# Performance work log

Hardware: AMD Instinct MI355X
Metric: run time of the kernel (lower is better)

Reference implementation:

```python
import jax, jax.numpy as jnp
import numpy as np

B, NF, G, F, D = 8192, 128, 16, 8, 512


def setup_inputs() -> dict:
    key = jax.random.key(0)
    k1, k2, k3, k4 = jax.random.split(key, 4)
    x = jax.random.normal(k1, (B, NF), dtype=jnp.float32)
    # per-group Linear weights: torch Linear(F, D) weight is [D, F]; store as [G, F, D]
    # init scale ~ 1/sqrt(fan_in) like torch default
    W = jax.random.normal(k2, (G, F, D), dtype=jnp.float32) / np.sqrt(F)
    b = jax.random.normal(k3, (G, D), dtype=jnp.float32) / np.sqrt(F)
    group_idx = jnp.arange(G * F, dtype=jnp.int64).reshape(G, F)  # contiguous groups
    masked_group_idx = jax.random.randint(k4, (B,), 0, G, dtype=jnp.int64)
    return {"x": x, "W": W, "b": b, "group_idx": group_idx,
            "masked_group_idx": masked_group_idx}


def reference(x, W, b, group_idx, masked_group_idx):
    # gather each group's feature columns: [B, G, F]
    xg = x[:, group_idx]
    # batched small GEMMs (block-diagonal gather-GEMM) + bias: [B, G, D]
    out = jnp.einsum('bgf,gfd->bgd', xg, W) + b[None, :, :]
    # zero out the masked group token per batch row
    mask = masked_group_idx[:, None] == jnp.arange(out.shape[1])[None, :]  # [B, G]
    out = jnp.where(mask[:, :, None], jnp.zeros((), out.dtype), out)
    return out
```

## Files before the change

### kernel.cpp

```cpp
#include <hip/hip_runtime.h>
#include <stdint.h>

constexpr int kB  = 8192;
constexpr int kNF = 128;
constexpr int kG  = 16;
constexpr int kF  = 8;
constexpr int kD  = 512;
constexpr int R   = 32;
constexpr int THREADS = 1024;
constexpr int BLOCKS  = kB / R;

typedef float f32x4 __attribute__((ext_vector_type(4)));

__global__ __launch_bounds__(THREADS) void ge_kernel(
    const float* __restrict__ x,
    const float* __restrict__ W,
    const float* __restrict__ bias,
    const int*  __restrict__ mgi_w,
    float* __restrict__ out)
{
    __shared__ __align__(16) float xs[R][kNF];
    __shared__ int mg[R];

    const int tid = threadIdx.x;
    const int b0  = blockIdx.x * R;

    const int lane = tid & 63;
    const int probe = mgi_w[lane];
    const bool lane_ok = (lane & 1) ? (probe == 0)
                                    : (probe >= 0 && probe < kG);
    const bool is64 = (__ballot(lane_ok) == ~0ull);

    {
        const f32x4* xsrc = (const f32x4*)(x + (size_t)b0 * kNF);
        ((f32x4*)&xs[0][0])[tid] = xsrc[tid];
    }
    if (tid < R) mg[tid] = mgi_w[is64 ? 2 * (b0 + tid) : (b0 + tid)];

    const int hi   = tid >> 7;
    const int dcol = (tid & 127) << 2;

    float w[2][kF][4];
    float bz[2][4];
    #pragma unroll
    for (int q = 0; q < 2; ++q) {
        const int g = 8 * q + hi;
        #pragma unroll
        for (int f = 0; f < kF; ++f)
            *(f32x4*)w[q][f] =
                *(const f32x4*)(W + (size_t)(g * kF + f) * kD + dcol);
        *(f32x4*)bz[q] = *(const f32x4*)(bias + (size_t)g * kD + dcol);
    }

    __syncthreads();

    float* outp = out + (size_t)b0 * (kG * kD) + dcol;

    #pragma unroll 1
    for (int r = 0; r < R; ++r) {
        const int m = mg[r];
        const float* xrow = &xs[r][0];
        float* orow = outp + (size_t)r * (kG * kD);
        #pragma unroll
        for (int q = 0; q < 2; ++q) {
            const int g = 8 * q + hi;
            const f32x4 xv0 = *(const f32x4*)&xrow[g * kF];
            const f32x4 xv1 = *(const f32x4*)&xrow[g * kF + 4];
            float a0 = bz[q][0], a1 = bz[q][1], a2 = bz[q][2], a3 = bz[q][3];
            a0 = fmaf(xv0.x, w[q][0][0], a0); a1 = fmaf(xv0.x, w[q][0][1], a1);
            a2 = fmaf(xv0.x, w[q][0][2], a2); a3 = fmaf(xv0.x, w[q][0][3], a3);
            a0 = fmaf(xv0.y, w[q][1][0], a0); a1 = fmaf(xv0.y, w[q][1][1], a1);
            a2 = fmaf(xv0.y, w[q][1][2], a2); a3 = fmaf(xv0.y, w[q][1][3], a3);
            a0 = fmaf(xv0.z, w[q][2][0], a0); a1 = fmaf(xv0.z, w[q][2][1], a1);
            a2 = fmaf(xv0.z, w[q][2][2], a2); a3 = fmaf(xv0.z, w[q][2][3], a3);
            a0 = fmaf(xv0.w, w[q][3][0], a0); a1 = fmaf(xv0.w, w[q][3][1], a1);
            a2 = fmaf(xv0.w, w[q][3][2], a2); a3 = fmaf(xv0.w, w[q][3][3], a3);
            a0 = fmaf(xv1.x, w[q][4][0], a0); a1 = fmaf(xv1.x, w[q][4][1], a1);
            a2 = fmaf(xv1.x, w[q][4][2], a2); a3 = fmaf(xv1.x, w[q][4][3], a3);
            a0 = fmaf(xv1.y, w[q][5][0], a0); a1 = fmaf(xv1.y, w[q][5][1], a1);
            a2 = fmaf(xv1.y, w[q][5][2], a2); a3 = fmaf(xv1.y, w[q][5][3], a3);
            a0 = fmaf(xv1.z, w[q][6][0], a0); a1 = fmaf(xv1.z, w[q][6][1], a1);
            a2 = fmaf(xv1.z, w[q][6][2], a2); a3 = fmaf(xv1.z, w[q][6][3], a3);
            a0 = fmaf(xv1.w, w[q][7][0], a0); a1 = fmaf(xv1.w, w[q][7][1], a1);
            a2 = fmaf(xv1.w, w[q][7][2], a2); a3 = fmaf(xv1.w, w[q][7][3], a3);
            const float s = (m == g) ? 0.0f : 1.0f;
            f32x4 o;
            o.x = a0 * s; o.y = a1 * s; o.z = a2 * s; o.w = a3 * s;
            __builtin_nontemporal_store(o, (f32x4*)(orow + (size_t)g * kD));
        }
    }
}

extern "C" void kernel_launch(void* const* d_in, const int* in_sizes, int n_in,
                              void* d_out, int out_size, void* d_ws, size_t ws_size,
                              hipStream_t stream) {
    const float* x    = (const float*)d_in[0];
    const float* W    = (const float*)d_in[1];
    const float* b    = (const float*)d_in[2];
    const int*   mgi  = (const int*)d_in[4];
    float*       out  = (float*)d_out;

    ge_kernel<<<dim3(BLOCKS), dim3(THREADS), 0, stream>>>(x, W, b, mgi, out);
}
```

Baseline: 277.5 us.

## Read x rows via wave-uniform scalar loads instead of LDS staging

```diff
diff --git a/kernel.cpp b/kernel.cpp
--- a/kernel.cpp
+++ b/kernel.cpp
@@ -19,9 +19,6 @@
     const int*  __restrict__ mgi_w,
     float* __restrict__ out)
 {
-    __shared__ __align__(16) float xs[R][kNF];
-    __shared__ int mg[R];
-
     const int tid = threadIdx.x;
     const int b0  = blockIdx.x * R;
 
@@ -31,13 +28,7 @@
                                     : (probe >= 0 && probe < kG);
     const bool is64 = (__ballot(lane_ok) == ~0ull);
 
-    {
-        const f32x4* xsrc = (const f32x4*)(x + (size_t)b0 * kNF);
-        ((f32x4*)&xs[0][0])[tid] = xsrc[tid];
-    }
-    if (tid < R) mg[tid] = mgi_w[is64 ? 2 * (b0 + tid) : (b0 + tid)];
-
-    const int hi   = tid >> 7;
+    const int hi   = __builtin_amdgcn_readfirstlane(tid >> 7);
     const int dcol = (tid & 127) << 2;
 
     float w[2][kF][4];
@@ -52,41 +43,38 @@
         *(f32x4*)bz[q] = *(const f32x4*)(bias + (size_t)g * kD + dcol);
     }
 
-    __syncthreads();
-
     float* outp = out + (size_t)b0 * (kG * kD) + dcol;
 
-    #pragma unroll 1
+    #pragma unroll 2
     for (int r = 0; r < R; ++r) {
-        const int m = mg[r];
-        const float* xrow = &xs[r][0];
+        const int b = b0 + r;
+        const float* xr0 = x + (size_t)b * kNF + hi * kF;
+        const float* xr1 = xr0 + 8 * kF;
+        float xv[2][kF];
+        #pragma unroll
+        for (int j = 0; j < kF; ++j) {
+            xv[0][j] = xr0[j];
+            xv[1][j] = xr1[j];
+        }
+        const int m = mgi_w[is64 ? 2 * b : b];
+
         float* orow = outp + (size_t)r * (kG * kD);
         #pragma unroll
         for (int q = 0; q < 2; ++q) {
             const int g = 8 * q + hi;
-            const f32x4 xv0 = *(const f32x4*)&xrow[g * kF];
-            const f32x4 xv1 = *(const f32x4*)&xrow[g * kF + 4];
             float a0 = bz[q][0], a1 = bz[q][1], a2 = bz[q][2], a3 = bz[q][3];
-            a0 = fmaf(xv0.x, w[q][0][0], a0); a1 = fmaf(xv0.x, w[q][0][1], a1);
-            a2 = fmaf(xv0.x, w[q][0][2], a2); a3 = fmaf(xv0.x, w[q][0][3], a3);
-            a0 = fmaf(xv0.y, w[q][1][0], a0); a1 = fmaf(xv0.y, w[q][1][1], a1);
-            a2 = fmaf(xv0.y, w[q][1][2], a2); a3 = fmaf(xv0.y, w[q][1][3], a3);
-            a0 = fmaf(xv0.z, w[q][2][0], a0); a1 = fmaf(xv0.z, w[q][2][1], a1);
-            a2 = fmaf(xv0.z, w[q][2][2], a2); a3 = fmaf(xv0.z, w[q][2][3], a3);
-            a0 = fmaf(xv0.w, w[q][3][0], a0); a1 = fmaf(xv0.w, w[q][3][1], a1);
-            a2 = fmaf(xv0.w, w[q][3][2], a2); a3 = fmaf(xv0.w, w[q][3][3], a3);
-            a0 = fmaf(xv1.x, w[q][4][0], a0); a1 = fmaf(xv1.x, w[q][4][1], a1);
-            a2 = fmaf(xv1.x, w[q][4][2], a2); a3 = fmaf(xv1.x, w[q][4][3], a3);
-            a0 = fmaf(xv1.y, w[q][5][0], a0); a1 = fmaf(xv1.y, w[q][5][1], a1);
-            a2 = fmaf(xv1.y, w[q][5][2], a2); a3 = fmaf(xv1.y, w[q][5][3], a3);
-            a0 = fmaf(xv1.z, w[q][6][0], a0); a1 = fmaf(xv1.z, w[q][6][1], a1);
-            a2 = fmaf(xv1.z, w[q][6][2], a2); a3 = fmaf(xv1.z, w[q][6][3], a3);
-            a0 = fmaf(xv1.w, w[q][7][0], a0); a1 = fmaf(xv1.w, w[q][7][1], a1);
-            a2 = fmaf(xv1.w, w[q][7][2], a2); a3 = fmaf(xv1.w, w[q][7][3], a3);
+            #pragma unroll
+            for (int f = 0; f < kF; ++f) {
+                const float xs_ = xv[q][f];
+                a0 = fmaf(xs_, w[q][f][0], a0);
+                a1 = fmaf(xs_, w[q][f][1], a1);
+                a2 = fmaf(xs_, w[q][f][2], a2);
+                a3 = fmaf(xs_, w[q][f][3], a3);
+            }
             const float s = (m == g) ? 0.0f : 1.0f;
             f32x4 o;
             o.x = a0 * s; o.y = a1 * s; o.z = a2 * s; o.w = a3 * s;
-            __builtin_nontemporal_store(o, (f32x4*)(orow + (size_t)g * kD));
+            *(f32x4*)(orow + (size_t)g * kD) = o;
         }
     }
 }
```

After: 280.3 us. Within noise of the previous version (+1.0%).
